# Performance work log

Measured on AMD Instinct MI355X. Metric: run time of the kernel, lower is better.

## Reference

```python
import jax, jax.numpy as jnp
import numpy as np

SEQ = 8192
DIM = 1280
NHEADS = 16
HEAD_DIM = DIM // NHEADS  # 80
NSEG = 8
SEG = SEQ // NSEG  # 1024


def setup_inputs() -> dict:
    key = jax.random.key(0)
    ks = jax.random.split(key, 7)
    hidden_states = jax.random.normal(ks[0], (SEQ, DIM), jnp.float32)
    # realistic rotary embeddings: cos/sin of random angles, shape [S, head_dim]
    ang = jax.random.uniform(ks[1], (SEQ, HEAD_DIM), jnp.float32, 0.0, 2.0 * np.pi)
    cos = jnp.cos(ang)
    sin = jnp.sin(ang)
    qkv_w = jax.random.normal(ks[2], (3 * DIM, DIM), jnp.float32) * (DIM ** -0.5)
    qkv_b = jax.random.normal(ks[3], (3 * DIM,), jnp.float32) * 0.02
    proj_w = jax.random.normal(ks[4], (DIM, DIM), jnp.float32) * (DIM ** -0.5)
    proj_b = jax.random.normal(ks[5], (DIM,), jnp.float32) * 0.02
    cu_seqlens = jnp.arange(NSEG + 1, dtype=jnp.int32) * SEG  # equal segments
    return {"hidden_states": hidden_states, "cos": cos, "sin": sin,
            "qkv_w": qkv_w, "qkv_b": qkv_b, "proj_w": proj_w, "proj_b": proj_b,
            "cu_seqlens": cu_seqlens}


def _rope(x, cos, sin):
    # x: [S, H, D]; cos/sin: [S, D] broadcast over heads. Computed in fp32.
    x = x.astype(jnp.float32)
    d = x.shape[-1]
    x1, x2 = x[..., : d // 2], x[..., d // 2:]
    rot = jnp.concatenate([-x2, x1], axis=-1)
    return x * cos[:, None, :] + rot * sin[:, None, :]


def reference(hidden_states, cos, sin, qkv_w, qkv_b, proj_w, proj_b, cu_seqlens):
    S, dim = hidden_states.shape
    nseg = cu_seqlens.shape[0] - 1
    seg = S // nseg  # segments are equal-length; block-diagonal attention batches over them
    H, D = NHEADS, dim // NHEADS

    qkv = hidden_states @ qkv_w.T + qkv_b                 # [S, 3*dim]
    qkv = qkv.reshape(S, 3, H, D)
    q, k, v = qkv[:, 0], qkv[:, 1], qkv[:, 2]             # [S, H, D]

    in_dtype = hidden_states.dtype
    q = _rope(q, cos, sin).astype(in_dtype)
    k = _rope(k, cos, sin).astype(in_dtype)

    scale = D ** -0.5
    qs = q.reshape(nseg, seg, H, D)
    ks = k.reshape(nseg, seg, H, D)
    vs = v.reshape(nseg, seg, H, D)

    scores = jnp.einsum('bqhd,bkhd->bhqk', qs, ks) * scale  # [nseg, H, seg, seg]
    probs = jax.nn.softmax(scores, axis=-1)
    out = jnp.einsum('bhqk,bkhd->bqhd', probs, vs)          # [nseg, seg, H, D]
    out = out.reshape(S, H * D)
    return out @ proj_w.T + proj_b
```

## Files before the change

### kernel.cpp

```cpp
#include <hip/hip_runtime.h>

#define SEQ 8192
#define DIM 1280
#define NHEADS 16
#define HD 80
#define HDP 96
#define NSEG 8
#define SEG 1024
#define KVB 64
#define NSTEP (SEG / KVB)
#define PST 72

typedef float f32x4 __attribute__((ext_vector_type(4)));
typedef short bf16x8 __attribute__((ext_vector_type(8)));
typedef unsigned int u32;

__device__ __forceinline__ float fast_exp2(float x) {
  return __builtin_amdgcn_exp2f(x);
}

__device__ __forceinline__ short f2bf(float f) {
  unsigned int u = __builtin_bit_cast(unsigned int, f);
  u = (u + 0x7fff + ((u >> 16) & 1)) >> 16;
  return (short)u;
}

__device__ __forceinline__ float bf2f(short s) {
  u32 u = ((u32)(unsigned short)s) << 16;
  return __builtin_bit_cast(float, u);
}

__device__ __forceinline__ u32 cvt_pk_bf16(float lo, float hi) {
  u32 r;
  asm("v_cvt_pk_bf16_f32 %0, %1, %2" : "=v"(r) : "v"(lo), "v"(hi));
  return r;
}

typedef __attribute__((address_space(1))) const unsigned int glds_src_t;
typedef __attribute__((address_space(3))) unsigned int glds_dst_t;
__device__ __forceinline__ void gload_lds16(const void* g, void* l) {
  __builtin_amdgcn_global_load_lds((glds_src_t*)g, (glds_dst_t*)l, 16, 0, 0);
}

__global__ void cast_f32_bf16(const float* __restrict__ in, short* __restrict__ out, int n) {
  int n4 = n >> 2;
  for (int i = blockIdx.x * blockDim.x + threadIdx.x; i < n4; i += gridDim.x * blockDim.x) {
    float4 v = ((const float4*)in)[i];
    short4 o;
    o.x = f2bf(v.x); o.y = f2bf(v.y); o.z = f2bf(v.z); o.w = f2bf(v.w);
    ((short4*)out)[i] = o;
  }
}

__global__ __launch_bounds__(512, 1) void gemm256(
    const short* __restrict__ A, const short* __restrict__ B,
    const float* __restrict__ bias, float* __restrict__ C,
    short* __restrict__ Cb, int M, int N, int K) {
  __shared__ short As[2][16384];
  __shared__ short Bs[2][16384];
  int tid = threadIdx.x;
  int w = tid >> 6, l = tid & 63;
  int lrow = l & 15, lg = l >> 4;
  int wm = w >> 2, wn = w & 3;
  int bid = blockIdx.x;
  int cpx = gridDim.x >> 3;
  int lid = (bid & 7) * cpx + (bid >> 3);
  int ntx = N >> 8;
  int m0 = (lid / ntx) * 256, n0 = (lid % ntx) * 256;

  const short* Ablk = A + (size_t)m0 * K;
  const short* Bblk = B + (size_t)n0 * K;

  f32x4 acc[8][4] = {};

#define STG_HALF(LDSB, GBASE, HALF, K0)                                       \
  {                                                                           \
    _Pragma("unroll") for (int rr = 0; rr < 2; rr++) {                        \
      int sb = rr * 512 + w * 64;                                             \
      int ss2 = sb + l;                                                       \
      int rl = ss2 >> 3, cc = ss2 & 7;                                        \
      int sl = cc ^ (rl & 7);                                                 \
      const short* sp = (GBASE) + (size_t)((HALF)*128 + rl) * K + (K0) + sl * 8; \
      gload_lds16(sp, (char*)(LDSB) + (HALF)*16384 + sb * 16);                \
    }                                                                         \
  }

#define LDA(MH, KS)                                                           \
  _Pragma("unroll") for (int mt = 0; mt < 4; mt++) {                          \
    int rowa = wm * 128 + ((MH)*4 + mt) * 16 + lrow;                          \
    int pa_ = ((KS)*4 + lg) ^ (rowa & 7);                                     \
    a[mt] = *(const bf16x8*)&As[cur][rowa * 64 + pa_ * 8];                    \
  }
#define LDB(KS)                                                               \
  _Pragma("unroll") for (int nt = 0; nt < 4; nt++) {                          \
    int rowb = wn * 64 + nt * 16 + lrow;                                      \
    int pb_ = ((KS)*4 + lg) ^ (rowb & 7);                                     \
    b[nt] = *(const bf16x8*)&Bs[cur][rowb * 64 + pb_ * 8];                    \
  }
#define MFMA16(MH)                                                            \
  _Pragma("unroll") for (int mt = 0; mt < 4; mt++)                            \
      _Pragma("unroll") for (int nt = 0; nt < 4; nt++)                        \
          acc[(MH)*4 + mt][nt] = __builtin_amdgcn_mfma_f32_16x16x32_bf16(     \
              a[mt], b[nt], acc[(MH)*4 + mt][nt], 0, 0, 0);
#define PHASE_SYNC()                                                          \
  __builtin_amdgcn_s_barrier();                                               \
  asm volatile("s_waitcnt lgkmcnt(0)" ::: "memory");                          \
  __builtin_amdgcn_sched_barrier(0);
#define PHASE_END()                                                           \
  __builtin_amdgcn_s_barrier();                                               \
  asm volatile("" ::: "memory");

  {
    short* Ad = &As[0][0];
    short* Bd = &Bs[0][0];
    STG_HALF(Ad, Ablk, 0, 0);
    STG_HALF(Ad, Ablk, 1, 0);
    STG_HALF(Bd, Bblk, 0, 0);
    STG_HALF(Bd, Bblk, 1, 0);
  }
  asm volatile("s_waitcnt vmcnt(0)" ::: "memory");
  __builtin_amdgcn_s_barrier();
  asm volatile("" ::: "memory");

  int NT = K >> 6;
  for (int t = 0; t < NT; ++t) {
    int cur = t & 1;
    int k1 = (t + 1) << 6;
    bool pre = (t + 1 < NT);
    short* Ad = &As[cur ^ 1][0];
    short* Bd = &Bs[cur ^ 1][0];
    bf16x8 a[4], b[4];
    LDA(0, 0); LDB(0);
    if (pre) { STG_HALF(Ad, Ablk, 0, k1); STG_HALF(Bd, Bblk, 0, k1); }
    PHASE_SYNC();
    __builtin_amdgcn_s_setprio(1); MFMA16(0); __builtin_amdgcn_s_setprio(0);
    PHASE_END();
    LDA(1, 0);
    if (pre) { STG_HALF(Ad, Ablk, 1, k1); STG_HALF(Bd, Bblk, 1, k1); }
    PHASE_SYNC();
    __builtin_amdgcn_s_setprio(1); MFMA16(1); __builtin_amdgcn_s_setprio(0);
    PHASE_END();
    LDA(0, 1); LDB(1);
    PHASE_SYNC();
    __builtin_amdgcn_s_setprio(1); MFMA16(0); __builtin_amdgcn_s_setprio(0);
    PHASE_END();
    LDA(1, 1);
    PHASE_SYNC();
    __builtin_amdgcn_s_setprio(1); MFMA16(1); __builtin_amdgcn_s_setprio(0);
    asm volatile("s_waitcnt vmcnt(0)" ::: "memory");
    PHASE_END();
  }

#pragma unroll
  for (int nt = 0; nt < 4; nt++) {
    int col = n0 + wn * 64 + nt * 16 + lrow;
    float bv = bias[col];
#pragma unroll
    for (int mt = 0; mt < 8; mt++) {
      int mrow = m0 + wm * 128 + mt * 16 + lg * 4;
      if (Cb) {
#pragma unroll
        for (int r = 0; r < 4; r++)
          Cb[(size_t)(mrow + r) * N + col] = f2bf(acc[mt][nt][r] + bv);
      } else {
#pragma unroll
        for (int r = 0; r < 4; r++)
          C[(size_t)(mrow + r) * N + col] = acc[mt][nt][r] + bv;
      }
    }
  }
#undef STG_HALF
#undef LDA
#undef LDB
#undef MFMA16
#undef PHASE_SYNC
#undef PHASE_END
}

__global__ __launch_bounds__(256) void gemm_bt_bias(
    const short* __restrict__ A, const short* __restrict__ B,
    const float* __restrict__ bias, float* __restrict__ C,
    short* __restrict__ Cb, int M, int N, int K) {
  __shared__ short As[2][128 * 64];
  __shared__ short Bs[2][128 * 64];
  int tid = threadIdx.x;
  int w = tid >> 6, l = tid & 63;
  int lrow = l & 15, lg = l >> 4;
  int bid = blockIdx.x;
  int cpx = gridDim.x >> 3;
  int lid = (bid & 7) * cpx + (bid >> 3);
  int ntx = N >> 7;
  int m0 = (lid / ntx) * 128, n0 = (lid % ntx) * 128;
  int wm = w & 1, wn = w >> 1;

  f32x4 acc[4][4] = {};

  const char* Abase = (const char*)A + (size_t)m0 * K * 2;
  const char* Bbase = (const char*)B + (size_t)n0 * K * 2;

#define STAGE_G(BUF, K0)                                                       \
  {                                                                            \
    _Pragma("unroll") for (int j = 0; j < 4; j++) {                            \
      int c = j * 256 + tid;                                                   \
      int row = c >> 3;                                                        \
      int slc = (c & 7) ^ (row & 7);                                           \
      size_t goff = (size_t)row * K * 2 + (size_t)(K0) * 2 + slc * 16;         \
      int loff = (j * 256 + w * 64) * 16;                                      \
      gload_lds16(Abase + goff, (char*)&As[BUF][0] + loff);                    \
      gload_lds16(Bbase + goff, (char*)&Bs[BUF][0] + loff);                    \
    }                                                                          \
  }

  STAGE_G(0, 0);
  asm volatile("s_waitcnt vmcnt(0)" ::: "memory");
  __builtin_amdgcn_s_barrier();
  asm volatile("" ::: "memory");

  for (int k0 = 0; k0 < K; k0 += 64) {
    int cur = (k0 >> 6) & 1;
    if (k0 + 64 < K) {
      STAGE_G(cur ^ 1, k0 + 64);
      asm volatile("s_waitcnt vmcnt(8)" ::: "memory");
    } else {
      asm volatile("s_waitcnt vmcnt(0)" ::: "memory");
    }
    __builtin_amdgcn_s_barrier();
    asm volatile("" ::: "memory");
#pragma unroll
    for (int kk = 0; kk < 2; kk++) {
      bf16x8 a[4], b[4];
#pragma unroll
      for (int mt = 0; mt < 4; mt++) {
        int row = wm * 64 + mt * 16 + lrow;
        int p = (kk * 4 + lg) ^ (row & 7);
        a[mt] = *(const bf16x8*)&As[cur][row * 64 + p * 8];
      }
#pragma unroll
      for (int nt = 0; nt < 4; nt++) {
        int row = wn * 64 + nt * 16 + lrow;
        int p = (kk * 4 + lg) ^ (row & 7);
        b[nt] = *(const bf16x8*)&Bs[cur][row * 64 + p * 8];
      }
#pragma unroll
      for (int mt = 0; mt < 4; mt++)
#pragma unroll
        for (int nt = 0; nt < 4; nt++)
          acc[mt][nt] = __builtin_amdgcn_mfma_f32_16x16x32_bf16(a[mt], b[nt], acc[mt][nt], 0, 0, 0);
    }
    __builtin_amdgcn_s_barrier();
    asm volatile("" ::: "memory");
  }

#pragma unroll
  for (int nt = 0; nt < 4; nt++) {
    int col = n0 + wn * 64 + nt * 16 + lrow;
    float bv = bias[col];
#pragma unroll
    for (int mt = 0; mt < 4; mt++) {
      int mrow = m0 + wm * 64 + mt * 16 + lg * 4;
      if (Cb) {
#pragma unroll
        for (int r = 0; r < 4; r++)
          Cb[(size_t)(mrow + r) * N + col] = f2bf(acc[mt][nt][r] + bv);
      } else {
#pragma unroll
        for (int r = 0; r < 4; r++)
          C[(size_t)(mrow + r) * N + col] = acc[mt][nt][r] + bv;
      }
    }
  }
}

__global__ void rope_qk(const short* __restrict__ qkv, const float* __restrict__ cosb,
                        const float* __restrict__ sinb, short* __restrict__ qg,
                        short* __restrict__ kg) {
  int t = blockIdx.x * blockDim.x + threadIdx.x;
  if (t >= SEQ * NHEADS * 40) return;
  int d = t % 40;
  int h = (t / 40) & 15;
  int s = t / 640;
  const short* row = qkv + (size_t)s * (3 * DIM);
  float c0 = cosb[s * HD + d], c1 = cosb[s * HD + d + 40];
  float s0 = sinb[s * HD + d], s1 = sinb[s * HD + d + 40];
  float x1 = bf2f(row[h * HD + d]), x2 = bf2f(row[h * HD + d + 40]);
  float q0 = x1 * c0 - x2 * s0;
  float q1 = x2 * c1 + x1 * s1;
  float y1 = bf2f(row[DIM + h * HD + d]), y2 = bf2f(row[DIM + h * HD + d + 40]);
  float k0 = y1 * c0 - y2 * s0;
  float k1 = y2 * c1 + y1 * s1;
  const float sc = 0.11180339887498949f * 1.4426950408889634f;
  size_t base = ((size_t)h * SEQ + s) * HDP;
  qg[base + d] = f2bf(q0 * sc);
  qg[base + d + 40] = f2bf(q1 * sc);
  kg[base + d] = f2bf(k0);
  kg[base + d + 40] = f2bf(k1);
  if (d < 16) { qg[base + 80 + d] = 0; kg[base + 80 + d] = 0; }
}

__global__ void v_transpose(const short* __restrict__ qkv, short* __restrict__ vt) {
  __shared__ short T[16][72];
  int st = blockIdx.x, dt = blockIdx.y, h = blockIdx.z;
  int d0 = dt * 16, s0 = st * 64;
  int t = threadIdx.x;
  int dd = t & 15, ss = t >> 4;
#pragma unroll
  for (int j = 0; j < 4; j++) {
    int s = ss + j * 16;
    T[dd][s] = qkv[(size_t)(s0 + s) * (3 * DIM) + 2 * DIM + h * HD + d0 + dd];
  }
  __syncthreads();
  int s2 = t & 63, dr = t >> 6;
#pragma unroll
  for (int j = 0; j < 4; j++) {
    int d = dr + j * 4;
    vt[((size_t)(h * HD + d0 + d)) * SEQ + s0 + s2] = T[d][s2];
  }
}

__global__ __launch_bounds__(512, 2) void attn_kernel(
    const short* __restrict__ qg, const short* __restrict__ kg,
    const short* __restrict__ vt, short* __restrict__ out) {
  __shared__ short Ks[2][64 * 128];
  __shared__ short Pl[8][32 * PST];
  int bid = blockIdx.x;
  int b = bid & 7, h = (bid >> 3) & 15, qt = bid >> 7;
  int tid = threadIdx.x;
  int w = tid >> 6, l = tid & 63;
  int lrow = l & 15, lg = l >> 4;
  int qbase_s = b * SEG + qt * 256 + w * 32;

  const short* qh = qg + (size_t)h * SEQ * HDP;
  const short* kh = kg + (size_t)h * SEQ * HDP;
  const short* vh = vt + (size_t)h * HD * SEQ;

#define STAGE_K(BUF, KEY0N)                                                    \
  {                                                                            \
    _Pragma("unroll") for (int sr = 0; sr < 2; sr++) {                         \
      int sbase = sr * 512 + w * 64;                                           \
      int ss = sbase + l;                                                      \
      int skey = ss >> 4, sc = ss & 15;                                        \
      int slc = sc ^ (skey & 7);                                               \
      const short* ssrc =                                                      \
          kh + (size_t)((KEY0N) + skey) * HDP + (slc < 12 ? slc * 8 : 0);      \
      gload_lds16(ssrc, (char*)&Ks[BUF][0] + sbase * 16);                      \
    }                                                                          \
  }

  bf16x8 qf[2][3];
#pragma unroll
  for (int mt = 0; mt < 2; mt++)
#pragma unroll
    for (int ks = 0; ks < 3; ks++)
      qf[mt][ks] = *(const bf16x8*)&qh[(size_t)(qbase_s + mt * 16 + lrow) * HDP + ks * 32 + lg * 8];

  f32x4 o[2][5] = {};
  float m_st[2] = {-1e30f, -1e30f};
  float l_st[2] = {0.f, 0.f};

  short* Pw = &Pl[w][0];

  STAGE_K(0, b * SEG);
  __syncthreads();

  for (int i = 0; i < NSTEP; i++) {
    int cur = i & 1;
    int key0 = b * SEG + i * KVB;
    if (i + 1 < NSTEP) {
      STAGE_K(cur ^ 1, key0 + KVB);
    }

    f32x4 sv[2][4] = {};
    __builtin_amdgcn_s_setprio(1);
#pragma unroll
    for (int kt = 0; kt < 4; kt++) {
      bf16x8 kf[3];
      int key = kt * 16 + lrow;
#pragma unroll
      for (int ks = 0; ks < 3; ks++) {
        int p = (ks * 4 + lg) ^ (key & 7);
        kf[ks] = *(const bf16x8*)&Ks[cur][key * 128 + p * 8];
      }
#pragma unroll
      for (int mt = 0; mt < 2; mt++)
#pragma unroll
        for (int ks = 0; ks < 3; ks++)
          sv[mt][kt] = __builtin_amdgcn_mfma_f32_16x16x32_bf16(kf[ks], qf[mt][ks], sv[mt][kt], 0, 0, 0);
    }
    __builtin_amdgcn_s_setprio(0);

    bf16x8 vf[5][2];
#pragma unroll
    for (int nt = 0; nt < 5; nt++)
#pragma unroll
      for (int ks = 0; ks < 2; ks++)
        vf[nt][ks] = *(const bf16x8*)&vh[(size_t)(nt * 16 + lrow) * SEQ + key0 + ks * 32 + lg * 8];

    float cm[2];
#pragma unroll
    for (int mt = 0; mt < 2; mt++) {
      float a0 = fmaxf(fmaxf(sv[mt][0][0], sv[mt][0][1]), fmaxf(sv[mt][0][2], sv[mt][0][3]));
      float a1 = fmaxf(fmaxf(sv[mt][1][0], sv[mt][1][1]), fmaxf(sv[mt][1][2], sv[mt][1][3]));
      float a2 = fmaxf(fmaxf(sv[mt][2][0], sv[mt][2][1]), fmaxf(sv[mt][2][2], sv[mt][2][3]));
      float a3 = fmaxf(fmaxf(sv[mt][3][0], sv[mt][3][1]), fmaxf(sv[mt][3][2], sv[mt][3][3]));
      float c = fmaxf(fmaxf(a0, a1), fmaxf(a2, a3));
      c = fmaxf(c, __shfl_xor(c, 16));
      c = fmaxf(c, __shfl_xor(c, 32));
      cm[mt] = c;
    }
    if (__any((cm[0] > m_st[0] + 8.f) || (cm[1] > m_st[1] + 8.f))) {
#pragma unroll
      for (int mt = 0; mt < 2; mt++) {
        float mn = fmaxf(m_st[mt], cm[mt]);
        float c = fast_exp2(m_st[mt] - mn);
        m_st[mt] = mn;
        l_st[mt] *= c;
        float cr[4];
#pragma unroll
        for (int r = 0; r < 4; r++) cr[r] = __shfl(c, lg * 4 + r);
#pragma unroll
        for (int nt = 0; nt < 5; nt++)
#pragma unroll
          for (int r = 0; r < 4; r++) o[mt][nt][r] *= cr[r];
      }
    }
#pragma unroll
    for (int mt = 0; mt < 2; mt++) {
      float rs = 0.f;
#pragma unroll
      for (int kt = 0; kt < 4; kt++) {
#pragma unroll
        for (int r = 0; r < 4; r++) {
          sv[mt][kt][r] = fast_exp2(sv[mt][kt][r] - m_st[mt]);
          rs += sv[mt][kt][r];
        }
        uint2 pk;
        pk.x = cvt_pk_bf16(sv[mt][kt][0], sv[mt][kt][1]);
        pk.y = cvt_pk_bf16(sv[mt][kt][2], sv[mt][kt][3]);
        *(uint2*)&Pw[(mt * 16 + lrow) * PST + kt * 16 + lg * 4] = pk;
      }
      rs += __shfl_xor(rs, 16);
      rs += __shfl_xor(rs, 32);
      l_st[mt] += rs;
    }

    bf16x8 pa[2][2];
#pragma unroll
    for (int mt = 0; mt < 2; mt++)
#pragma unroll
      for (int ks = 0; ks < 2; ks++)
        pa[mt][ks] = *(const bf16x8*)&Pw[(mt * 16 + lrow) * PST + ks * 32 + lg * 8];
    __builtin_amdgcn_s_setprio(1);
#pragma unroll
    for (int nt = 0; nt < 5; nt++)
#pragma unroll
      for (int mt = 0; mt < 2; mt++)
#pragma unroll
        for (int ks = 0; ks < 2; ks++)
          o[mt][nt] = __builtin_amdgcn_mfma_f32_16x16x32_bf16(pa[mt][ks], vf[nt][ks], o[mt][nt], 0, 0, 0);
    __builtin_amdgcn_s_setprio(0);

    __syncthreads();
  }

#pragma unroll
  for (int mt = 0; mt < 2; mt++) {
    float rl = 1.f / l_st[mt];
    float ir[4];
#pragma unroll
    for (int r = 0; r < 4; r++) ir[r] = __shfl(rl, lg * 4 + r);
#pragma unroll
    for (int r = 0; r < 4; r++) {
      int srow = qbase_s + mt * 16 + lg * 4 + r;
#pragma unroll
      for (int nt = 0; nt < 5; nt++)
        out[(size_t)srow * DIM + h * HD + nt * 16 + lrow] = f2bf(o[mt][nt][r] * ir[r]);
    }
  }
}

extern "C" void kernel_launch(void* const* d_in, const int* in_sizes, int n_in,
                              void* d_out, int out_size, void* d_ws, size_t ws_size,
                              hipStream_t stream) {
  const float* hidden = (const float*)d_in[0];
  const float* cosb = (const float*)d_in[1];
  const float* sinb = (const float*)d_in[2];
  const float* qkv_w = (const float*)d_in[3];
  const float* qkv_b = (const float*)d_in[4];
  const float* proj_w = (const float*)d_in[5];
  const float* proj_b = (const float*)d_in[6];

  char* ws = (char*)d_ws;
  short* qkv_bf = (short*)(ws);
  short* attn_o = (short*)(ws);
  short* wp_bf = (short*)(ws + 23068672);
  short* q_bf = (short*)(ws + 125829120);
  short* k_bf = (short*)(ws + 150994944);
  short* v_tb = (short*)(ws + 176160768);
  short* h_bf = (short*)(ws + 197132288);
  short* wq_bf = (short*)(ws + 218103808);

  cast_f32_bf16<<<4096, 256, 0, stream>>>(hidden, h_bf, SEQ * DIM);
  cast_f32_bf16<<<4096, 256, 0, stream>>>(qkv_w, wq_bf, 3 * DIM * DIM);
  gemm256<<<480, 512, 0, stream>>>(h_bf, wq_bf, qkv_b, nullptr, qkv_bf, SEQ, 3 * DIM, DIM);
  rope_qk<<<20480, 256, 0, stream>>>(qkv_bf, cosb, sinb, q_bf, k_bf);
  v_transpose<<<dim3(128, 5, 16), 256, 0, stream>>>(qkv_bf, v_tb);
  cast_f32_bf16<<<2048, 256, 0, stream>>>(proj_w, wp_bf, DIM * DIM);
  attn_kernel<<<512, 512, 0, stream>>>(q_bf, k_bf, v_tb, attn_o);
  gemm_bt_bias<<<640, 256, 0, stream>>>(attn_o, wp_bf, proj_b, (float*)d_out, nullptr, SEQ, DIM, DIM);
}
```

Measured before the change: 317.1 us.

## Simplify 256-tile GEMM pipeline and stage bf16 epilogue through LDS

Replaces the four-phase, barrier-per-phase main loop of the 256x256 GEMM with a single prefetch of the next K-tile, a partial vmcnt wait, and one barrier pair around all LDS reads and MFMAs of the current tile. The bf16 output path now writes results into LDS in 64-row slices and copies them out with coalesced 16-byte stores instead of scattered 2-byte stores. The goal is fewer barriers per K-step and better write coalescing. In exchange, global loads may overlap less with MFMA work than in the finer-grained phase schedule, and the epilogue adds extra LDS traffic and syncs.

```diff
diff --git a/kernel.cpp b/kernel.cpp
--- a/kernel.cpp
+++ b/kernel.cpp
@@ -84,7 +84,6 @@
       gload_lds16(sp, (char*)(LDSB) + (HALF)*16384 + sb * 16);                \
     }                                                                         \
   }
-
 #define LDA(MH, KS)                                                           \
   _Pragma("unroll") for (int mt = 0; mt < 4; mt++) {                          \
     int rowa = wm * 128 + ((MH)*4 + mt) * 16 + lrow;                          \
@@ -102,13 +101,6 @@
       _Pragma("unroll") for (int nt = 0; nt < 4; nt++)                        \
           acc[(MH)*4 + mt][nt] = __builtin_amdgcn_mfma_f32_16x16x32_bf16(     \
               a[mt], b[nt], acc[(MH)*4 + mt][nt], 0, 0, 0);
-#define PHASE_SYNC()                                                          \
-  __builtin_amdgcn_s_barrier();                                               \
-  asm volatile("s_waitcnt lgkmcnt(0)" ::: "memory");                          \
-  __builtin_amdgcn_sched_barrier(0);
-#define PHASE_END()                                                           \
-  __builtin_amdgcn_s_barrier();                                               \
-  asm volatile("" ::: "memory");
 
   {
     short* Ad = &As[0][0];
@@ -125,44 +117,69 @@
   int NT = K >> 6;
   for (int t = 0; t < NT; ++t) {
     int cur = t & 1;
-    int k1 = (t + 1) << 6;
-    bool pre = (t + 1 < NT);
-    short* Ad = &As[cur ^ 1][0];
-    short* Bd = &Bs[cur ^ 1][0];
-    bf16x8 a[4], b[4];
-    LDA(0, 0); LDB(0);
-    if (pre) { STG_HALF(Ad, Ablk, 0, k1); STG_HALF(Bd, Bblk, 0, k1); }
-    PHASE_SYNC();
-    __builtin_amdgcn_s_setprio(1); MFMA16(0); __builtin_amdgcn_s_setprio(0);
-    PHASE_END();
-    LDA(1, 0);
-    if (pre) { STG_HALF(Ad, Ablk, 1, k1); STG_HALF(Bd, Bblk, 1, k1); }
-    PHASE_SYNC();
-    __builtin_amdgcn_s_setprio(1); MFMA16(1); __builtin_amdgcn_s_setprio(0);
-    PHASE_END();
-    LDA(0, 1); LDB(1);
-    PHASE_SYNC();
-    __builtin_amdgcn_s_setprio(1); MFMA16(0); __builtin_amdgcn_s_setprio(0);
-    PHASE_END();
-    LDA(1, 1);
-    PHASE_SYNC();
-    __builtin_amdgcn_s_setprio(1); MFMA16(1); __builtin_amdgcn_s_setprio(0);
-    asm volatile("s_waitcnt vmcnt(0)" ::: "memory");
-    PHASE_END();
-  }
-
-#pragma unroll
-  for (int nt = 0; nt < 4; nt++) {
-    int col = n0 + wn * 64 + nt * 16 + lrow;
-    float bv = bias[col];
-#pragma unroll
-    for (int mt = 0; mt < 8; mt++) {
-      int mrow = m0 + wm * 128 + mt * 16 + lg * 4;
-      if (Cb) {
-#pragma unroll
-        for (int r = 0; r < 4; r++)
-          Cb[(size_t)(mrow + r) * N + col] = f2bf(acc[mt][nt][r] + bv);
-      } else {
+    if (t + 1 < NT) {
+      short* Ad = &As[cur ^ 1][0];
+      short* Bd = &Bs[cur ^ 1][0];
+      int k1 = (t + 1) << 6;
+      STG_HALF(Ad, Ablk, 0, k1);
+      STG_HALF(Ad, Ablk, 1, k1);
+      STG_HALF(Bd, Bblk, 0, k1);
+      STG_HALF(Bd, Bblk, 1, k1);
+      asm volatile("s_waitcnt vmcnt(8)" ::: "memory");
+    } else {
+      asm volatile("s_waitcnt vmcnt(0)" ::: "memory");
+    }
+    __builtin_amdgcn_s_barrier();
+    asm volatile("" ::: "memory");
+    {
+      bf16x8 a[4], b[4];
+      __builtin_amdgcn_s_setprio(1);
+      LDA(0, 0); LDB(0); MFMA16(0);
+      LDA(1, 0); MFMA16(1);
+      LDA(0, 1); LDB(1); MFMA16(0);
+      LDA(1, 1); MFMA16(1);
+      __builtin_amdgcn_s_setprio(0);
+    }
+    __builtin_amdgcn_s_barrier();
+    asm volatile("" ::: "memory");
+  }
+
+  if (Cb) {
+    short* E = &As[0][0];
+#pragma unroll
+    for (int s = 0; s < 4; s++) {
+      __syncthreads();
+      if (wm == (s >> 1)) {
+#pragma unroll
+        for (int mi = 0; mi < 4; mi++) {
+          int mt2 = (s & 1) * 4 + mi;
+#pragma unroll
+          for (int nt = 0; nt < 4; nt++) {
+            int col = wn * 64 + nt * 16 + lrow;
+            float bv = bias[n0 + col];
+#pragma unroll
+            for (int r = 0; r < 4; r++)
+              E[(mi * 16 + lg * 4 + r) * 264 + col] = f2bf(acc[mt2][nt][r] + bv);
+          }
+        }
+      }
+      __syncthreads();
+#pragma unroll
+      for (int j = 0; j < 4; j++) {
+        int c = j * 512 + tid;
+        int row = c >> 5, ch = c & 31;
+        *(uint4*)&Cb[(size_t)(m0 + s * 64 + row) * N + n0 + ch * 8] =
+            *(const uint4*)&E[row * 264 + ch * 8];
+      }
+    }
+  } else {
+#pragma unroll
+    for (int nt = 0; nt < 4; nt++) {
+      int col = n0 + wn * 64 + nt * 16 + lrow;
+      float bv = bias[col];
+#pragma unroll
+      for (int mt = 0; mt < 8; mt++) {
+        int mrow = m0 + wm * 128 + mt * 16 + lg * 4;
 #pragma unroll
         for (int r = 0; r < 4; r++)
           C[(size_t)(mrow + r) * N + col] = acc[mt][nt][r] + bv;
@@ -173,8 +190,6 @@
 #undef LDA
 #undef LDB
 #undef MFMA16
-#undef PHASE_SYNC
-#undef PHASE_END
 }
 
 __global__ __launch_bounds__(256) void gemm_bt_bias(
```

Measured after the change: 313.2 us. No clear change (-1.2%).
